# Kernel tuning notes

Hardware: AMD Instinct MI355X
Metric: run time of the kernel (lower is better)

The kernel has to match this reference:

```python
import jax, jax.numpy as jnp
import numpy as np
from jax import lax

B, T, H, L, LAT, OUT, NH = 4096, 60, 512, 2, 128, 14, 4
EPS = 1e-5


def _ln(x, g, b):
    m = x.mean(-1, keepdims=True)
    v = ((x - m) ** 2).mean(-1, keepdims=True)
    return (x - m) / jnp.sqrt(v + EPS) * g + b


def setup_inputs() -> dict:
    key = jax.random.key(0)
    ks = jax.random.split(key, 24)
    f32 = jnp.float32
    def rn(k, shape, s=0.05):
        return jax.random.normal(k, shape, dtype=f32) * s
    return {
        'x': jax.random.normal(ks[0], (B, T, 17), dtype=f32),
        'conv1_w': rn(ks[1], (24, 9, 3)), 'conv1_b': rn(ks[2], (24,)),
        'bn1_g': jnp.ones(24, f32), 'bn1_b': jnp.zeros(24, f32),
        'bn1_rm': rn(ks[3], (24,), 0.1), 'bn1_rv': jnp.full((24,), 0.8, f32),
        'comp_w': rn(ks[4], (20, 8)), 'comp_b': rn(ks[5], (20,)),
        'proj_w': rn(ks[6], (H, 44)), 'proj_b': rn(ks[7], (H,)),
        'gates_w': rn(ks[8], (L, 5, H, 2 * H), 0.02), 'gates_b': rn(ks[9], (L, 5, H)),
        'retention': jnp.full((L, H), 0.9, f32),
        'expln_g': jnp.ones((L, H), f32), 'expln_b': jnp.zeros((L, H), f32),
        'ln_g': jnp.ones((L, H), f32), 'ln_b': jnp.zeros((L, H), f32),
        'attn_in_w': rn(ks[10], (3 * H, H), 0.02), 'attn_in_b': rn(ks[11], (3 * H,)),
        'attn_out_w': rn(ks[12], (H, H), 0.02), 'attn_out_b': rn(ks[13], (H,)),
        'bneck_w': rn(ks[14], (LAT, H)), 'bneck_b': rn(ks[15], (LAT,)),
        'bn2_g': jnp.ones(LAT, f32), 'bn2_b': jnp.zeros(LAT, f32),
        'bn2_rm': rn(ks[16], (LAT,), 0.1), 'bn2_rv': jnp.full((LAT,), 0.9, f32),
        'out_w': rn(ks[17], (OUT, LAT)), 'out_b': rn(ks[18], (OUT,)),
    }


def _forward(x, conv1_w, conv1_b, bn1_g, bn1_b, bn1_rm, bn1_rv, comp_w, comp_b,
             proj_w, proj_b, gates_w, gates_b, retention, expln_g, expln_b,
             ln_g, ln_b, attn_in_w, attn_in_b, attn_out_w, attn_out_b,
             bneck_w, bneck_b, bn2_g, bn2_b, bn2_rm, bn2_rv, out_w, out_b):
    bsz = x.shape[0]
    hd = proj_w.shape[0]
    nlayers = gates_w.shape[0]
    # --- conv branch on relative features (eval-mode BatchNorm) ---
    rel = x[:, :, :9].transpose(0, 2, 1)                      # [B,9,T]
    y = lax.conv_general_dilated(rel, conv1_w, (1,), [(1, 1)],
                                 dimension_numbers=('NCH', 'OIH', 'NCH'))
    y = jax.nn.relu(y + conv1_b[None, :, None])
    y = (y - bn1_rm[None, :, None]) / jnp.sqrt(bn1_rv + EPS)[None, :, None] \
        * bn1_g[None, :, None] + bn1_b[None, :, None]
    th = y.shape[2] // 2
    y = y[:, :, :th * 2].reshape(bsz, 24, th, 2).max(-1)      # MaxPool1d(2)
    rel_feat = y.transpose(0, 2, 1)                           # [B,30,24]
    # --- company embedding branch ---
    comp = jax.nn.relu(x[:, :30, 9:] @ comp_w.T + comp_b)     # [B,30,20]
    combined = jnp.concatenate([rel_feat, comp], -1) @ proj_w.T + proj_b  # [B,30,H]
    # --- stacked xLSTM over time ---
    h0 = jnp.zeros((nlayers, bsz, hd), x.dtype)
    c0 = jnp.zeros((nlayers, bsz, hd), x.dtype)
    def step(carry, x_t):
        h, c = carry
        inp = x_t
        hs, cs = [], []
        for l in range(nlayers):
            comb = jnp.concatenate([inp, h[l]], -1)           # [B,2H]
            g = jnp.einsum('bk,ghk->gbh', comb, gates_w[l]) + gates_b[l][:, None, :]
            f = jax.nn.sigmoid(g[0]); i = jax.nn.sigmoid(g[1])
            o = jax.nn.sigmoid(g[2]); cc = jnp.tanh(g[3]); m = jax.nn.sigmoid(g[4])
            r = retention[l]
            c_new = f * c[l] + i * cc
            c_new = c_new * r + (1 - r) * c[l]
            c_new = m * c_new + (1 - m) * c[l]
            o_exp = jax.nn.sigmoid(_ln(o, expln_g[l], expln_b[l]))  # exp(z)/(1+exp(z))
            h_new = _ln(o_exp * jnp.tanh(c_new), ln_g[l], ln_b[l])
            hs.append(h_new); cs.append(c_new)
            inp = h_new
        return (jnp.stack(hs), jnp.stack(cs)), inp
    _, seq = lax.scan(step, (h0, c0), combined.transpose(1, 0, 2))
    seq = seq.transpose(1, 0, 2)                              # [B,30,H]
    # --- multi-head self attention (eval, 4 heads) ---
    dh = hd // NH
    qkv = seq @ attn_in_w.T + attn_in_b
    q, k, v = jnp.split(qkv, 3, axis=-1)
    q = q.reshape(bsz, -1, NH, dh); k = k.reshape(bsz, -1, NH, dh); v = v.reshape(bsz, -1, NH, dh)
    scores = jnp.einsum('bqhd,bkhd->bhqk', q, k) / jnp.sqrt(jnp.float32(dh))
    attn = jnp.einsum('bhqk,bkhd->bqhd', jax.nn.softmax(scores, -1), v)
    attn = attn.reshape(bsz, -1, hd) @ attn_out_w.T + attn_out_b
    final = attn[:, -1, :]
    latent = final @ bneck_w.T + bneck_b
    latent = (latent - bn2_rm) / jnp.sqrt(bn2_rv + EPS) * bn2_g + bn2_b
    return latent @ out_w.T + out_b


def reference(x, conv1_w, conv1_b, bn1_g, bn1_b, bn1_rm, bn1_rv, comp_w, comp_b,
              proj_w, proj_b, gates_w, gates_b, retention, expln_g, expln_b,
              ln_g, ln_b, attn_in_w, attn_in_b, attn_out_w, attn_out_b,
              bneck_w, bneck_b, bn2_g, bn2_b, bn2_rm, bn2_rv, out_w, out_b):
    return _forward(x, conv1_w, conv1_b, bn1_g, bn1_b, bn1_rm, bn1_rv, comp_w, comp_b,
                    proj_w, proj_b, gates_w, gates_b, retention, expln_g, expln_b,
                    ln_g, ln_b, attn_in_w, attn_in_b, attn_out_w, attn_out_b,
                    bneck_w, bneck_b, bn2_g, bn2_b, bn2_rm, bn2_rv, out_w, out_b)
```

## Files before the change

### kernel.cpp

```cpp
#include <hip/hip_runtime.h>
#include <hip/hip_bf16.h>
#include <hip/hip_fp16.h>

#define B_   4096
#define T_   60
#define TT   30
#define H_   512
#define L_   2
#define NH_  4
#define DH_  128
#define LAT_ 128
#define OUT_ 14
#define NGATE_ (5*H_)
#define EPSF 1e-5f
#define FEATK 64
#define K0M  (FEATK + H_)

typedef __attribute__((ext_vector_type(8))) short bf16x8;
typedef __attribute__((ext_vector_type(4))) short sh4;
typedef __attribute__((ext_vector_type(4))) float f32x4;

__device__ __forceinline__ float sigmoidf_(float x) { return 1.0f / (1.0f + __expf(-x)); }
__device__ __forceinline__ float bf2f(short s) {
    return __uint_as_float(((unsigned)(unsigned short)s) << 16);
}

__device__ __forceinline__ void async_load16(const void* g, void* l) {
    __builtin_amdgcn_global_load_lds((const __attribute__((address_space(1))) void*)g,
                                     (__attribute__((address_space(3))) void*)l, 16, 0, 0);
}

__device__ __forceinline__ int perm_row(int n) {
    int g = n >> 9, j = n & 511;
    return (j >> 4) * 80 + g * 16 + (j & 15);
}

__global__ __launch_bounds__(256) void cvt_bf16(const float* __restrict__ in,
                                                __hip_bfloat16* __restrict__ out, long n) {
    long i = (long)blockIdx.x * blockDim.x + threadIdx.x;
    long stride = (long)gridDim.x * blockDim.x;
    for (; i < n; i += stride) out[i] = __float2bfloat16(in[i]);
}

__global__ __launch_bounds__(256) void zero_f32(float* __restrict__ p, long n) {
    long i = (long)blockIdx.x * blockDim.x + threadIdx.x;
    long stride = (long)gridDim.x * blockDim.x;
    for (; i < n; i += stride) p[i] = 0.0f;
}

__global__ __launch_bounds__(256)
void perm_w1(const float* __restrict__ gw, __hip_bfloat16* __restrict__ w1p) {
    long i = (long)blockIdx.x * 256 + threadIdx.x;
    if (i >= (long)NGATE_ * 2 * H_) return;
    int n = (int)(i >> 10), k = (int)(i & 1023);
    w1p[(long)perm_row(n) * (2 * H_) + k] = __float2bfloat16(gw[i]);
}

__global__ __launch_bounds__(256)
void build_w0m(const float* __restrict__ gw, const float* __restrict__ pw,
               const float* __restrict__ pb, const float* __restrict__ gb,
               __hip_bfloat16* __restrict__ w0p, float* __restrict__ bc) {
    const int tid = threadIdx.x;
    const int n = blockIdx.x * 4 + (tid >> 6);
    const int f = tid & 63;
    const long np = perm_row(n);
    const float* wrow = gw + (long)n * (2 * H_);
    float acc = 0.f;
    if (f < 44) {
        for (int k = 0; k < H_; ++k) acc += wrow[k] * pw[k * 44 + f];
    }
    w0p[np * K0M + f] = __float2bfloat16(acc);
    #pragma unroll
    for (int j = 0; j < 8; ++j) {
        int col = f * 8 + j;
        w0p[np * K0M + FEATK + col] = __float2bfloat16(wrow[H_ + col]);
    }
    float s = 0.f;
    #pragma unroll
    for (int j = 0; j < 8; ++j) s += wrow[f * 8 + j] * pb[f * 8 + j];
    #pragma unroll
    for (int off = 32; off > 0; off >>= 1) s += __shfl_down(s, off, 64);
    if (f == 0) bc[n] = gb[n] + s;
}

__global__ __launch_bounds__(256)
void build_wkd(const float* __restrict__ aiw, __hip_bfloat16* __restrict__ wkd) {
    int i = blockIdx.x * 256 + threadIdx.x;
    if (i >= 2048 * 512) return;
    int n = i >> 9, k = i & 511;
    float v = ((k >> 7) == (n >> 9)) ? aiw[(H_ + k) * H_ + (n & 511)] : 0.f;
    wkd[i] = __float2bfloat16(v);
}

__global__ __launch_bounds__(256)
void build_wvd(const float* __restrict__ aiw, __hip_bfloat16* __restrict__ wvd) {
    int i = blockIdx.x * 256 + threadIdx.x;
    if (i >= 512 * 2048) return;
    int n = i >> 11, k = i & 2047;
    float v = ((k >> 9) == (n >> 7)) ? aiw[(2 * H_ + n) * H_ + (k & 511)] : 0.f;
    wvd[i] = __float2bfloat16(v);
}

__global__ __launch_bounds__(256)
void frontend_kernel(const float* __restrict__ x,
                     const float* __restrict__ cw, const float* __restrict__ cb,
                     const float* __restrict__ bg, const float* __restrict__ bb,
                     const float* __restrict__ brm, const float* __restrict__ brv,
                     const float* __restrict__ compw, const float* __restrict__ compb,
                     __hip_bfloat16* __restrict__ feat_out) {
    const int b = blockIdx.x, tid = threadIdx.x;
    __shared__ float xs[T_ * 17];
    __shared__ float ybuf[24][T_];
    __shared__ float feat[TT][44];

    for (int i = tid; i < T_ * 17; i += 256) xs[i] = x[(long)b * T_ * 17 + i];
    __syncthreads();

    for (int i = tid; i < 24 * T_; i += 256) {
        int oc = i / T_, t = i % T_;
        float acc = cb[oc];
        #pragma unroll
        for (int kk = 0; kk < 3; ++kk) {
            int tt = t + kk - 1;
            if (tt >= 0 && tt < T_) {
                #pragma unroll
                for (int ic = 0; ic < 9; ++ic)
                    acc += xs[tt * 17 + ic] * cw[(oc * 9 + ic) * 3 + kk];
            }
        }
        acc = fmaxf(acc, 0.f);
        acc = (acc - brm[oc]) * rsqrtf(brv[oc] + EPSF) * bg[oc] + bb[oc];
        ybuf[oc][t] = acc;
    }
    __syncthreads();

    for (int i = tid; i < TT * 24; i += 256) {
        int u = i / 24, oc = i % 24;
        feat[u][oc] = fmaxf(ybuf[oc][2 * u], ybuf[oc][2 * u + 1]);
    }
    for (int i = tid; i < TT * 20; i += 256) {
        int u = i / 20, oc = i % 20;
        float acc = compb[oc];
        #pragma unroll
        for (int j = 0; j < 8; ++j) acc += xs[u * 17 + 9 + j] * compw[oc * 8 + j];
        feat[u][24 + oc] = fmaxf(acc, 0.f);
    }
    __syncthreads();

    for (int i = tid; i < TT * FEATK; i += 256) {
        int u = i >> 6, c = i & 63;
        float v = (c < 44) ? feat[u][c] : 0.f;
        feat_out[((long)b * TT + u) * FEATK + c] = __float2bfloat16(v);
    }
}

template <int WRITE_BF16>
__device__ __forceinline__
void gemm_core(const __hip_bfloat16* __restrict__ A0, int lda0,
               const __hip_bfloat16* __restrict__ A1, int lda1, int ksplit,
               const __hip_bfloat16* __restrict__ W, int ldw,
               const float* __restrict__ bias,
               void* __restrict__ Cout, int ldc, int K, int bx, int by) {
    __shared__ __hip_bfloat16 As[128 * 64];
    __shared__ __hip_bfloat16 Bs[128 * 64];
    const int tid = threadIdx.x;
    const int wave = tid >> 6, lane = tid & 63;
    const long m0 = (long)by * 128;
    const long n0 = (long)bx * 128;

    f32x4 acc[4][4] = {};

    for (int k0 = 0; k0 < K; k0 += 64) {
        __syncthreads();
        #pragma unroll
        for (int it = 0; it < 4; ++it) {
            int id = it * 256 + tid;
            int row = id >> 3;
            int kc = ((id & 7) ^ (row & 7)) << 3;
            int gk = k0 + kc;
            const __hip_bfloat16* srcA;
            if (gk < ksplit) srcA = A0 + (m0 + row) * (long)lda0 + gk;
            else             srcA = A1 + (m0 + row) * (long)lda1 + (gk - ksplit);
            async_load16(srcA, &As[id * 8]);
            const __hip_bfloat16* srcB = W + (n0 + row) * (long)ldw + gk;
            async_load16(srcB, &Bs[id * 8]);
        }
        __syncthreads();
        #pragma unroll
        for (int ks = 0; ks < 2; ++ks) {
            const int kb = ((ks * 4 + (lane >> 4)) ^ (lane & 7)) << 3;
            const int ar = (wave >> 1) * 64 + (lane & 15);
            const int br = (wave & 1) * 64 + (lane & 15);
            bf16x8 afr[4], bfr[4];
            #pragma unroll
            for (int i = 0; i < 4; ++i) afr[i] = *(const bf16x8*)&As[(ar + i * 16) * 64 + kb];
            #pragma unroll
            for (int i = 0; i < 4; ++i) bfr[i] = *(const bf16x8*)&Bs[(br + i * 16) * 64 + kb];
            #pragma unroll
            for (int mi = 0; mi < 4; ++mi)
                #pragma unroll
                for (int ni = 0; ni < 4; ++ni)
                    acc[mi][ni] = __builtin_amdgcn_mfma_f32_16x16x32_bf16(afr[mi], bfr[ni], acc[mi][ni], 0, 0, 0);
        }
    }

    const int cr = (lane >> 4) * 4;
    const int ccol = lane & 15;
    #pragma unroll
    for (int ni = 0; ni < 4; ++ni) {
        long col = n0 + (wave & 1) * 64 + ni * 16 + ccol;
        float bv = bias ? bias[col] : 0.f;
        #pragma unroll
        for (int mi = 0; mi < 4; ++mi) {
            long rowb = m0 + (wave >> 1) * 64 + mi * 16 + cr;
            #pragma unroll
            for (int r = 0; r < 4; ++r) {
                float v = acc[mi][ni][r] + bv;
                if (WRITE_BF16)
                    ((__hip_bfloat16*)Cout)[(rowb + r) * (long)ldc + col] = __float2bfloat16(v);
                else
                    ((float*)Cout)[(rowb + r) * (long)ldc + col] = v;
            }
        }
    }
}

template <int WRITE_BF16>
__global__ __launch_bounds__(256)
void gemm_bias(const __hip_bfloat16* __restrict__ A0, int lda0,
               const __hip_bfloat16* __restrict__ A1, int lda1, int ksplit,
               const __hip_bfloat16* __restrict__ W, int ldw,
               const float* __restrict__ bias,
               void* __restrict__ Cout, int ldc, int K) {
    gemm_core<WRITE_BF16>(A0, lda0, A1, lda1, ksplit, W, ldw, bias, Cout, ldc, K,
                          blockIdx.x, blockIdx.y);
}

__device__ __forceinline__
void fused_gate_core(const __hip_bfloat16* __restrict__ A0, int lda0,
                     const __hip_bfloat16* __restrict__ A1, int lda1,
                     int ksplit, int K,
                     const __hip_bfloat16* __restrict__ Wp, int ldw,
                     const float* __restrict__ bias,
                     const float* __restrict__ ret,
                     float* __restrict__ c_t,
                     __half* __restrict__ opre,
                     __half* __restrict__ tcn,
                     int m, int nblk) {
    __shared__ __hip_bfloat16 As[2][128 * 64];
    __shared__ __hip_bfloat16 Bs[2][80 * 64];
    const int tid = threadIdx.x;
    const int wave = tid >> 6, lane = tid & 63;
    const long m0 = (long)m * 128;
    const int n0row = nblk * 80;
    const int jbase = nblk * 16;
    const int rsel = lane & 15;
    const int q = lane >> 4;

    const int kc = ((tid & 7) ^ ((tid >> 3) & 7)) << 3;
    const int srow = tid >> 3;
    const __hip_bfloat16* pA0_t = A0 + (m0 + srow) * (long)lda0 + kc;
    const __hip_bfloat16* pA1_t =
        A1 ? (A1 + (m0 + srow) * (long)lda1 + kc - ksplit) : pA0_t;
    const __hip_bfloat16* pB_t = Wp + (long)(n0row + srow) * ldw + kc;
    const int ks_slab = ksplit >> 6;
    const int nslab = K >> 6;

    auto stage = [&](int hb, int kk) {
        const long koff = (long)kk << 6;
        const __hip_bfloat16* pa;
        long la;
        if (kk < ks_slab) { pa = pA0_t; la = lda0; }
        else              { pa = pA1_t; la = lda1; }
        #pragma unroll
        for (int it = 0; it < 4; ++it)
            async_load16(pa + (long)it * 32 * la + koff,
                         &As[hb][it * 2048 + tid * 8]);
        #pragma unroll
        for (int it = 0; it < 2; ++it)
            async_load16(pB_t + (long)it * 32 * ldw + koff,
                         &Bs[hb][it * 2048 + tid * 8]);
        if (tid < 128)
            async_load16(pB_t + (long)64 * ldw + koff,
                         &Bs[hb][4096 + tid * 8]);
    };

    stage(0, 0);
    f32x4 acc[2][5] = {};

    for (int kk = 0; kk < nslab; ++kk) {
        const int hb = kk & 1;
        __syncthreads();
        if (kk + 1 < nslab) stage(hb ^ 1, kk + 1);
        #pragma unroll
        for (int ks = 0; ks < 2; ++ks) {
            const int kb = ((ks * 4 + q) ^ (lane & 7)) << 3;
            bf16x8 afr[2], bfr[5];
            #pragma unroll
            for (int i = 0; i < 2; ++i)
                afr[i] = *(const bf16x8*)&As[hb][(wave * 32 + i * 16 + rsel) * 64 + kb];
            #pragma unroll
            for (int i = 0; i < 5; ++i)
                bfr[i] = *(const bf16x8*)&Bs[hb][(i * 16 + rsel) * 64 + kb];
            #pragma unroll
            for (int mi = 0; mi < 2; ++mi)
                #pragma unroll
                for (int ni = 0; ni < 5; ++ni)
                    acc[mi][ni] = __builtin_amdgcn_mfma_f32_16x16x32_bf16(bfr[ni], afr[mi], acc[mi][ni], 0, 0, 0);
        }
    }

    #pragma unroll
    for (int mi = 0; mi < 2; ++mi) {
        const long b = m0 + wave * 32 + mi * 16 + rsel;
        sh4 ov, tv;
        #pragma unroll
        for (int r = 0; r < 4; ++r) {
            const int jg = jbase + 4 * q + r;
            float f  = sigmoidf_(acc[mi][0][r] + bias[jg]);
            float ii = sigmoidf_(acc[mi][1][r] + bias[512 + jg]);
            float o  = sigmoidf_(acc[mi][2][r] + bias[1024 + jg]);
            float cc = tanhf(acc[mi][3][r] + bias[1536 + jg]);
            float mg = sigmoidf_(acc[mi][4][r] + bias[2048 + jg]);
            float cold = c_t[(long)jg * B_ + b];
            float rr = ret[jg];
            float cn = f * cold + ii * cc;
            cn = cn * rr + (1.f - rr) * cold;
            cn = mg * cn + (1.f - mg) * cold;
            c_t[(long)jg * B_ + b] = cn;
            __half oh = __float2half(o);
            __half th = __float2half(tanhf(cn));
            ov[r] = *(short*)&oh;
            tv[r] = *(short*)&th;
        }
        *(sh4*)&opre[b * H_ + jbase + 4 * q] = ov;
        *(sh4*)&tcn [b * H_ + jbase + 4 * q] = tv;
    }
}

__global__ __launch_bounds__(256)
void fused_gate_single(const __hip_bfloat16* A0, int lda0, const __hip_bfloat16* A1,
                       int lda1, int ksplit, int K,
                       const __hip_bfloat16* Wp, int ldw,
                       const float* bias, const float* ret, float* c_t,
                       __half* opre, __half* tcn) {
    const int id = blockIdx.x;
    const int xcd = id & 7;
    const int rest = id >> 3;
    const int m = xcd * 4 + (rest & 3);
    const int n = (rest >> 2) & 31;
    fused_gate_core(A0, lda0, A1, lda1, ksplit, K, Wp, ldw, bias, ret, c_t,
                    opre, tcn, m, n);
}

__global__ __launch_bounds__(256)
void fused_gate_dual(const __hip_bfloat16* A0a, int lda0a, const __hip_bfloat16* A1a,
                     int lda1a, int ksplita, int Ka,
                     const __hip_bfloat16* Wpa, int ldwa,
                     const float* biasa, const float* reta, float* cta,
                     __half* oprea, __half* tcna,
                     const __hip_bfloat16* A0b, int lda0b, const __hip_bfloat16* A1b,
                     int lda1b, int ksplitb, int Kb,
                     const __hip_bfloat16* Wpb, int ldwb,
                     const float* biasb, const float* retb, float* ctb,
                     __half* opreb, __half* tcnb) {
    const int id = blockIdx.x;
    const int xcd = id & 7;
    const int rest = id >> 3;
    const int m = xcd * 4 + (rest & 3);
    const int n = (rest >> 2) & 31;
    const int z = rest >> 7;
    if (z == 0)
        fused_gate_core(A0a, lda0a, A1a, lda1a, ksplita, Ka, Wpa, ldwa,
                        biasa, reta, cta, oprea, tcna, m, n);
    else
        fused_gate_core(A0b, lda0b, A1b, lda1b, ksplitb, Kb, Wpb, ldwb,
                        biasb, retb, ctb, opreb, tcnb, m, n);
}

__device__ __forceinline__ void block_reduce2(float& a, float& b, float* red) {
    #pragma unroll
    for (int off = 32; off > 0; off >>= 1) {
        a += __shfl_down(a, off, 64);
        b += __shfl_down(b, off, 64);
    }
    int lane = threadIdx.x & 63, w = threadIdx.x >> 6;
    if (lane == 0) { red[w] = a; red[8 + w] = b; }
    __syncthreads();
    a = red[0] + red[1] + red[2] + red[3];
    b = red[8] + red[9] + red[10] + red[11];
    __syncthreads();
}

__device__ __forceinline__
void gate_ln_body(const __half* __restrict__ opre,
                  const __half* __restrict__ tcn,
                  const float* __restrict__ elg, const float* __restrict__ elb,
                  const float* __restrict__ lng, const float* __restrict__ lnb,
                  __hip_bfloat16* __restrict__ hout, long hstride, int b) {
    const int tid = threadIdx.x;
    __shared__ float red[16];

    float o_[2], t_[2];
    float s = 0.f, s2 = 0.f;
    #pragma unroll
    for (int u = 0; u < 2; ++u) {
        int j = tid + u * 256;
        float o = __half2float(opre[(long)b * H_ + j]);
        float t = __half2float(tcn[(long)b * H_ + j]);
        o_[u] = o; t_[u] = t;
        s += o; s2 += o * o;
    }
    block_reduce2(s, s2, red);
    float mean = s * (1.f / H_);
    float var = s2 * (1.f / H_) - mean * mean;
    float rstd = rsqrtf(var + EPSF);

    float val[2];
    float s3 = 0.f, s4 = 0.f;
    #pragma unroll
    for (int u = 0; u < 2; ++u) {
        int j = tid + u * 256;
        float on = (o_[u] - mean) * rstd * elg[j] + elb[j];
        float v = sigmoidf_(on) * t_[u];
        val[u] = v; s3 += v; s4 += v * v;
    }
    block_reduce2(s3, s4, red);
    float mean2 = s3 * (1.f / H_);
    float var2 = s4 * (1.f / H_) - mean2 * mean2;
    float rstd2 = rsqrtf(var2 + EPSF);
    #pragma unroll
    for (int u = 0; u < 2; ++u) {
        int j = tid + u * 256;
        float h = (val[u] - mean2) * rstd2 * lng[j] + lnb[j];
        hout[(long)b * hstride + j] = __float2bfloat16(h);
    }
}

__global__ __launch_bounds__(256)
void gate_ln(const __half* __restrict__ opre,
             const __half* __restrict__ tcn,
             const float* __restrict__ elg, const float* __restrict__ elb,
             const float* __restrict__ lng, const float* __restrict__ lnb,
             __hip_bfloat16* __restrict__ hout, long hstride) {
    gate_ln_body(opre, tcn, elg, elb, lng, lnb, hout, hstride, blockIdx.x);
}

__global__ __launch_bounds__(256)
void gate_ln_dual(const __half* oa, const __half* ta,
                  const float* elga, const float* elba,
                  const float* lnga, const float* lnba,
                  __hip_bfloat16* houta, long hstridea,
                  const __half* ob, const __half* tb,
                  const float* elgb, const float* elbb,
                  const float* lngb, const float* lnbb,
                  __hip_bfloat16* houtb, long hstrideb) {
    int bid = blockIdx.x;
    bool isB = bid >= B_;
    int b = isB ? bid - B_ : bid;
    gate_ln_body(isB ? ob : oa, isB ? tb : ta,
                 isB ? elgb : elga, isB ? elbb : elba,
                 isB ? lngb : lnga, isB ? lnbb : lnba,
                 isB ? houtb : houta, isB ? hstrideb : hstridea, b);
}

__global__ __launch_bounds__(256)
void attn_fused(const __hip_bfloat16* __restrict__ seq,
                const __hip_bfloat16* __restrict__ U,
                __hip_bfloat16* __restrict__ sbar) {
    const int b = blockIdx.x, tid = threadIdx.x;
    const int h = tid >> 6, lane = tid & 63;
    const int c0 = lane * 8;
    __shared__ float ps[NH_ * TT];
    const float scale = 0.08838834764831845f;

    float uq[8];
    {
        bf16x8 uv = *(const bf16x8*)&U[(size_t)b * (NH_ * H_) + h * H_ + c0];
        for (int j = 0; j < 8; ++j) uq[j] = bf2f(uv[j]);
    }
    const __hip_bfloat16* srow = seq + (size_t)b * TT * H_;

    for (int t = 0; t < TT; ++t) {
        bf16x8 sv = *(const bf16x8*)&srow[t * H_ + c0];
        float a = 0.f;
        for (int j = 0; j < 8; ++j) a += uq[j] * bf2f(sv[j]);
        a += __shfl_xor(a, 32);
        a += __shfl_xor(a, 16);
        a += __shfl_xor(a, 8);
        a += __shfl_xor(a, 4);
        a += __shfl_xor(a, 2);
        a += __shfl_xor(a, 1);
        if (lane == 0) ps[h * TT + t] = a * scale;
    }
    __syncthreads();

    float mx = -1e30f;
    for (int t = 0; t < TT; ++t) mx = fmaxf(mx, ps[h * TT + t]);
    float den = 0.f;
    for (int t = 0; t < TT; ++t) den += __expf(ps[h * TT + t] - mx);
    float inv = 1.f / den;

    float accv[8];
    for (int j = 0; j < 8; ++j) accv[j] = 0.f;
    for (int t = 0; t < TT; ++t) {
        float w = __expf(ps[h * TT + t] - mx) * inv;
        bf16x8 sv = *(const bf16x8*)&srow[t * H_ + c0];
        for (int j = 0; j < 8; ++j) accv[j] += w * bf2f(sv[j]);
    }
    bf16x8 outv;
    for (int j = 0; j < 8; ++j) {
        __hip_bfloat16 hv = __float2bfloat16(accv[j]);
        outv[j] = *(short*)&hv;
    }
    *(bf16x8*)&sbar[(size_t)b * (NH_ * H_) + h * H_ + c0] = outv;
}

__global__ __launch_bounds__(128)
void head_kernel(const float* __restrict__ lat_in,
                 const float* __restrict__ g2, const float* __restrict__ b2,
                 const float* __restrict__ rm2, const float* __restrict__ rv2,
                 const float* __restrict__ ow, const float* __restrict__ ob,
                 float* __restrict__ out) {
    const int b = blockIdx.x, tid = threadIdx.x;
    __shared__ float ls[LAT_];
    float a = lat_in[(long)b * LAT_ + tid];
    ls[tid] = (a - rm2[tid]) * rsqrtf(rv2[tid] + EPSF) * g2[tid] + b2[tid];
    __syncthreads();
    if (tid < OUT_) {
        float acc = ob[tid];
        #pragma unroll 4
        for (int j = 0; j < LAT_; ++j) acc += ls[j] * ow[tid * LAT_ + j];
        out[(long)b * OUT_ + tid] = acc;
    }
}

extern "C" void kernel_launch(void* const* d_in, const int* in_sizes, int n_in,
                              void* d_out, int out_size, void* d_ws, size_t ws_size,
                              hipStream_t stream) {
    const float* x        = (const float*)d_in[0];
    const float* conv1_w  = (const float*)d_in[1];
    const float* conv1_b  = (const float*)d_in[2];
    const float* bn1_g    = (const float*)d_in[3];
    const float* bn1_b    = (const float*)d_in[4];
    const float* bn1_rm   = (const float*)d_in[5];
    const float* bn1_rv   = (const float*)d_in[6];
    const float* comp_w   = (const float*)d_in[7];
    const float* comp_b   = (const float*)d_in[8];
    const float* proj_w   = (const float*)d_in[9];
    const float* proj_b   = (const float*)d_in[10];
    const float* gates_w  = (const float*)d_in[11];
    const float* gates_b  = (const float*)d_in[12];
    const float* retention= (const float*)d_in[13];
    const float* expln_g  = (const float*)d_in[14];
    const float* expln_b  = (const float*)d_in[15];
    const float* ln_g     = (const float*)d_in[16];
    const float* ln_b     = (const float*)d_in[17];
    const float* attn_in_w  = (const float*)d_in[18];
    const float* attn_in_b  = (const float*)d_in[19];
    const float* attn_out_w = (const float*)d_in[20];
    const float* attn_out_b = (const float*)d_in[21];
    const float* bneck_w  = (const float*)d_in[22];
    const float* bneck_b  = (const float*)d_in[23];
    const float* bn2_g    = (const float*)d_in[24];
    const float* bn2_b    = (const float*)d_in[25];
    const float* bn2_rm   = (const float*)d_in[26];
    const float* bn2_rv   = (const float*)d_in[27];
    const float* out_w    = (const float*)d_in[28];
    const float* out_b    = (const float*)d_in[29];
    float* out = (float*)d_out;

    char* base = (char*)d_ws;
    size_t off = 0;
    auto alloc = [&](size_t nbytes) -> char* {
        char* p = base + off;
        off += (nbytes + 255) & ~(size_t)255;
        return p;
    };
    __hip_bfloat16* seq_bf = (__hip_bfloat16*)alloc((size_t)B_ * TT * H_ * 2);
    size_t g_bytes = (size_t)B_ * NGATE_ * 2;
    char* un = alloc(2 * g_bytes);
    __half* opreA = (__half*)un;
    __half* tcnA  = (__half*)(un + (size_t)4 * 1024 * 1024);
    __half* opreB = (__half*)(un + (size_t)8 * 1024 * 1024);
    __half* tcnB  = (__half*)(un + (size_t)12 * 1024 * 1024);
    __hip_bfloat16* U_bf    = (__hip_bfloat16*)un;
    __hip_bfloat16* sbar_bf = (__hip_bfloat16*)(un + (size_t)16 * 1024 * 1024);
    __hip_bfloat16* wkd_bf  = (__hip_bfloat16*)(un + (size_t)32 * 1024 * 1024);
    __hip_bfloat16* wvd_bf  = (__hip_bfloat16*)(un + (size_t)35 * 1024 * 1024);
    __hip_bfloat16* feat_bf = (__hip_bfloat16*)alloc((size_t)B_ * TT * FEATK * 2);
    float*          c0t   = (float*)alloc((size_t)B_ * H_ * 4);
    float*          c1t   = (float*)alloc((size_t)B_ * H_ * 4);
    __hip_bfloat16* h0_bf = (__hip_bfloat16*)alloc((size_t)B_ * H_ * 2);
    __hip_bfloat16* q_bf  = (__hip_bfloat16*)alloc((size_t)B_ * H_ * 2);
    __hip_bfloat16* fin_bf = q_bf;
    __hip_bfloat16* av_bf = (__hip_bfloat16*)alloc((size_t)B_ * H_ * 2);
    float*          lat_f = (float*)alloc((size_t)B_ * LAT_ * 4);
    __hip_bfloat16* w1p_bf = (__hip_bfloat16*)alloc((size_t)NGATE_ * 2 * H_ * 2);
    __hip_bfloat16* w0p_bf = (__hip_bfloat16*)alloc((size_t)NGATE_ * K0M * 2);
    float*          bc_f  = (float*)alloc((size_t)NGATE_ * 4);
    __hip_bfloat16* ai_bf = (__hip_bfloat16*)alloc((size_t)H_ * H_ * 2);
    __hip_bfloat16* ao_bf = (__hip_bfloat16*)alloc((size_t)H_ * H_ * 2);
    __hip_bfloat16* bw_bf = (__hip_bfloat16*)alloc((size_t)LAT_ * H_ * 2);
    (void)ws_size; (void)in_sizes; (void)n_in; (void)out_size;

    const int WL = 5 * H_ * 2 * H_;
    perm_w1<<<(NGATE_ * 2 * H_) / 256, 256, 0, stream>>>(gates_w + WL, w1p_bf);
    build_w0m<<<NGATE_ / 4, 256, 0, stream>>>(gates_w, proj_w, proj_b, gates_b,
                                              w0p_bf, bc_f);
    cvt_bf16<<<256, 256, 0, stream>>>(attn_in_w, ai_bf, (long)H_ * H_);
    cvt_bf16<<<256, 256, 0, stream>>>(attn_out_w, ao_bf, (long)H_ * H_);
    cvt_bf16<<<64, 256, 0, stream>>>(bneck_w, bw_bf, (long)LAT_ * H_);
    zero_f32<<<2048, 256, 0, stream>>>(c0t, (long)2 * B_ * H_);

    frontend_kernel<<<B_, 256, 0, stream>>>(x, conv1_w, conv1_b, bn1_g, bn1_b, bn1_rm,
                                            bn1_rv, comp_w, comp_b, feat_bf);

    fused_gate_single<<<1024, 256, 0, stream>>>(
        feat_bf, TT * FEATK, (const __hip_bfloat16*)nullptr, 0, FEATK, FEATK,
        w0p_bf, K0M, bc_f, retention, c0t, opreB, tcnB);
    gate_ln<<<B_, 256, 0, stream>>>(opreB, tcnB, expln_g, expln_b,
                                    ln_g, ln_b, h0_bf, H_);

    for (int t = 0; t < TT - 1; ++t) {
        fused_gate_dual<<<2048, 256, 0, stream>>>(
            h0_bf, H_, (t == 0) ? (const __hip_bfloat16*)nullptr
                                : seq_bf + (size_t)(t - 1) * H_,
            TT * H_, H_, (t == 0) ? H_ : 2 * H_,
            w1p_bf, 2 * H_, gates_b + NGATE_, retention + H_, c1t, opreA, tcnA,
            feat_bf + (size_t)(t + 1) * FEATK, TT * FEATK, h0_bf, H_, FEATK, K0M,
            w0p_bf, K0M, bc_f, retention, c0t, opreB, tcnB);
        gate_ln_dual<<<2 * B_, 256, 0, stream>>>(
            opreA, tcnA, expln_g + H_, expln_b + H_, ln_g + H_, ln_b + H_,
            seq_bf + (size_t)t * H_, TT * H_,
            opreB, tcnB, expln_g, expln_b, ln_g, ln_b, h0_bf, H_);
    }
    fused_gate_single<<<1024, 256, 0, stream>>>(
        h0_bf, H_, seq_bf + (size_t)(TT - 2) * H_, TT * H_, H_, 2 * H_,
        w1p_bf, 2 * H_, gates_b + NGATE_, retention + H_, c1t, opreA, tcnA);
    gate_ln<<<B_, 256, 0, stream>>>(opreA, tcnA, expln_g + H_, expln_b + H_,
                                    ln_g + H_, ln_b + H_,
                                    seq_bf + (size_t)(TT - 1) * H_, TT * H_);

    build_wkd<<<4096, 256, 0, stream>>>(attn_in_w, wkd_bf);
    build_wvd<<<4096, 256, 0, stream>>>(attn_in_w, wvd_bf);

    gemm_bias<1><<<dim3(H_ / 128, B_ / 128), 256, 0, stream>>>(
        seq_bf + (size_t)29 * H_, TT * H_, (const __hip_bfloat16*)nullptr, 0, H_,
        ai_bf, H_, attn_in_b, (void*)q_bf, H_, H_);

    gemm_bias<1><<<dim3(2048 / 128, B_ / 128), 256, 0, stream>>>(
        q_bf, H_, (const __hip_bfloat16*)nullptr, 0, H_,
        wkd_bf, H_, (const float*)nullptr, (void*)U_bf, 2048, H_);

    attn_fused<<<B_, 256, 0, stream>>>(seq_bf, U_bf, sbar_bf);

    gemm_bias<1><<<dim3(H_ / 128, B_ / 128), 256, 0, stream>>>(
        sbar_bf, 2048, (const __hip_bfloat16*)nullptr, 0, 2048,
        wvd_bf, 2048, attn_in_b + 2 * H_, (void*)av_bf, H_, 2048);

    gemm_bias<1><<<dim3(H_ / 128, B_ / 128), 256, 0, stream>>>(
        av_bf, H_, (const __hip_bfloat16*)nullptr, 0, H_,
        ao_bf, H_, attn_out_b, (void*)fin_bf, H_, H_);

    gemm_bias<0><<<dim3(LAT_ / 128, B_ / 128), 256, 0, stream>>>(
        fin_bf, H_, (const __hip_bfloat16*)nullptr, 0, H_,
        bw_bf, H_, bneck_b, (void*)lat_f, LAT_, H_);
    head_kernel<<<B_, 128, 0, stream>>>(lat_f, bn2_g, bn2_b, bn2_rm, bn2_rv,
                                        out_w, out_b, out);
}
```

Baseline: 2.443 ms.

## Replace block-diagonal attention weight GEMMs with per-head GEMMs and stage sequence in LDS

The K and V projections previously ran as dense GEMMs over block-diagonal weight matrices that were mostly zeros. They now run as four per-head GEMMs with compact weights, which removes the zero-block FLOPs and shrinks the weight-building kernels. The attention kernel now loads the whole per-batch sequence into shared memory with async loads and precomputes the softmax weights once, instead of reading global memory twice and recomputing exp. The cost is more kernel launches, small grids for the V GEMMs (32 blocks each), and 30 KB of LDS per block, which can reduce occupancy.

```diff
diff --git a/kernel.cpp b/kernel.cpp
--- a/kernel.cpp
+++ b/kernel.cpp
@@ -84,21 +84,13 @@
 }
 
 __global__ __launch_bounds__(256)
-void build_wkd(const float* __restrict__ aiw, __hip_bfloat16* __restrict__ wkd) {
+void build_wkt(const float* __restrict__ aiw, __hip_bfloat16* __restrict__ wkt) {
     int i = blockIdx.x * 256 + threadIdx.x;
-    if (i >= 2048 * 512) return;
-    int n = i >> 9, k = i & 511;
-    float v = ((k >> 7) == (n >> 9)) ? aiw[(H_ + k) * H_ + (n & 511)] : 0.f;
-    wkd[i] = __float2bfloat16(v);
-}
-
-__global__ __launch_bounds__(256)
-void build_wvd(const float* __restrict__ aiw, __hip_bfloat16* __restrict__ wvd) {
-    int i = blockIdx.x * 256 + threadIdx.x;
-    if (i >= 512 * 2048) return;
-    int n = i >> 11, k = i & 2047;
-    float v = ((k >> 9) == (n >> 7)) ? aiw[(2 * H_ + n) * H_ + (k & 511)] : 0.f;
-    wvd[i] = __float2bfloat16(v);
+    if (i >= 2048 * 128) return;
+    int row = i >> 7;
+    int k = i & 127;
+    int h = row >> 9, j = row & 511;
+    wkt[i] = __float2bfloat16(aiw[(H_ + h * 128 + k) * H_ + j]);
 }
 
 __global__ __launch_bounds__(256)
@@ -471,18 +463,24 @@
     const int b = blockIdx.x, tid = threadIdx.x;
     const int h = tid >> 6, lane = tid & 63;
     const int c0 = lane * 8;
+    __shared__ __hip_bfloat16 ss[TT * H_];
     __shared__ float ps[NH_ * TT];
+    __shared__ float we[NH_ * TT];
     const float scale = 0.08838834764831845f;
+
+    const __hip_bfloat16* srow = seq + (size_t)b * TT * H_;
+    for (int i = tid; i < TT * H_ / 8; i += 256)
+        async_load16(srow + i * 8, &ss[i * 8]);
 
     float uq[8];
     {
         bf16x8 uv = *(const bf16x8*)&U[(size_t)b * (NH_ * H_) + h * H_ + c0];
         for (int j = 0; j < 8; ++j) uq[j] = bf2f(uv[j]);
     }
-    const __hip_bfloat16* srow = seq + (size_t)b * TT * H_;
+    __syncthreads();
 
     for (int t = 0; t < TT; ++t) {
-        bf16x8 sv = *(const bf16x8*)&srow[t * H_ + c0];
+        bf16x8 sv = *(const bf16x8*)&ss[t * H_ + c0];
         float a = 0.f;
         for (int j = 0; j < 8; ++j) a += uq[j] * bf2f(sv[j]);
         a += __shfl_xor(a, 32);
@@ -500,12 +498,14 @@
     float den = 0.f;
     for (int t = 0; t < TT; ++t) den += __expf(ps[h * TT + t] - mx);
     float inv = 1.f / den;
+    if (lane < TT) we[h * TT + lane] = __expf(ps[h * TT + lane] - mx) * inv;
+    __syncthreads();
 
     float accv[8];
     for (int j = 0; j < 8; ++j) accv[j] = 0.f;
     for (int t = 0; t < TT; ++t) {
-        float w = __expf(ps[h * TT + t] - mx) * inv;
-        bf16x8 sv = *(const bf16x8*)&srow[t * H_ + c0];
+        float w = we[h * TT + t];
+        bf16x8 sv = *(const bf16x8*)&ss[t * H_ + c0];
         for (int j = 0; j < 8; ++j) accv[j] += w * bf2f(sv[j]);
     }
     bf16x8 outv;
@@ -586,8 +586,8 @@
     __half* tcnB  = (__half*)(un + (size_t)12 * 1024 * 1024);
     __hip_bfloat16* U_bf    = (__hip_bfloat16*)un;
     __hip_bfloat16* sbar_bf = (__hip_bfloat16*)(un + (size_t)16 * 1024 * 1024);
-    __hip_bfloat16* wkd_bf  = (__hip_bfloat16*)(un + (size_t)32 * 1024 * 1024);
-    __hip_bfloat16* wvd_bf  = (__hip_bfloat16*)(un + (size_t)35 * 1024 * 1024);
+    __hip_bfloat16* wkt_bf  = (__hip_bfloat16*)(un + (size_t)32 * 1024 * 1024);
+    __hip_bfloat16* wv_bf   = (__hip_bfloat16*)(un + (size_t)35 * 1024 * 1024);
     __hip_bfloat16* feat_bf = (__hip_bfloat16*)alloc((size_t)B_ * TT * FEATK * 2);
     float*          c0t   = (float*)alloc((size_t)B_ * H_ * 4);
     float*          c1t   = (float*)alloc((size_t)B_ * H_ * 4);
@@ -642,22 +642,27 @@
                                     ln_g + H_, ln_b + H_,
                                     seq_bf + (size_t)(TT - 1) * H_, TT * H_);
 
-    build_wkd<<<4096, 256, 0, stream>>>(attn_in_w, wkd_bf);
-    build_wvd<<<4096, 256, 0, stream>>>(attn_in_w, wvd_bf);
+    build_wkt<<<1024, 256, 0, stream>>>(attn_in_w, wkt_bf);
+    cvt_bf16<<<1024, 256, 0, stream>>>(attn_in_w + (size_t)(2 * H_) * H_, wv_bf,
+                                       (long)H_ * H_);
 
     gemm_bias<1><<<dim3(H_ / 128, B_ / 128), 256, 0, stream>>>(
         seq_bf + (size_t)29 * H_, TT * H_, (const __hip_bfloat16*)nullptr, 0, H_,
         ai_bf, H_, attn_in_b, (void*)q_bf, H_, H_);
 
-    gemm_bias<1><<<dim3(2048 / 128, B_ / 128), 256, 0, stream>>>(
-        q_bf, H_, (const __hip_bfloat16*)nullptr, 0, H_,
-        wkd_bf, H_, (const float*)nullptr, (void*)U_bf, 2048, H_);
+    for (int h = 0; h < NH_; ++h)
+        gemm_bias<1><<<dim3(4, B_ / 128), 256, 0, stream>>>(
+            q_bf + h * DH_, H_, (const __hip_bfloat16*)nullptr, 0, DH_,
+            wkt_bf + (size_t)h * 512 * DH_, DH_, (const float*)nullptr,
+            (void*)(U_bf + h * 512), 2048, DH_);
 
     attn_fused<<<B_, 256, 0, stream>>>(seq_bf, U_bf, sbar_bf);
 
-    gemm_bias<1><<<dim3(H_ / 128, B_ / 128), 256, 0, stream>>>(
-        sbar_bf, 2048, (const __hip_bfloat16*)nullptr, 0, 2048,
-        wvd_bf, 2048, attn_in_b + 2 * H_, (void*)av_bf, H_, 2048);
+    for (int h = 0; h < NH_; ++h)
+        gemm_bias<1><<<dim3(1, B_ / 128), 256, 0, stream>>>(
+            sbar_bf + h * 512, 2048, (const __hip_bfloat16*)nullptr, 0, H_,
+            wv_bf + (size_t)h * DH_ * H_, H_, attn_in_b + 2 * H_ + h * DH_,
+            (void*)(av_bf + h * DH_), H_, H_);
 
     gemm_bias<1><<<dim3(H_ / 128, B_ / 128), 256, 0, stream>>>(
         av_bf, H_, (const __hip_bfloat16*)nullptr, 0, H_,
```

Result: no change. 2.439 ms (median of 2 runs) (-0.2%).
